# Performance work log

Hardware: AMD Instinct MI355X
Metric: run time of the kernel (lower is better)

The kernel has to match this reference:

```python
import jax, jax.numpy as jnp
import numpy as np

B, T, C = 8, 2048, 1024
H, S = 16, 64  # heads, head size (R=K=V=S)
HEAD_SIZE_DIVISOR = 8.0
EPS = 1e-5


def setup_inputs() -> dict:
    key = jax.random.key(0)
    ks = jax.random.split(key, 16)
    n = lambda k, shape, s=1.0: jax.random.normal(k, shape, dtype=jnp.float32) * s
    u = lambda k, shape: jax.random.uniform(k, shape, dtype=jnp.float32)
    w_scale = 0.02
    return {
        "xq": n(ks[0], (B, T, C)),
        "xk": n(ks[1], (B, T, C)),
        "xv": n(ks[2], (B, T, C)),
        "time_mix_k": u(ks[3], (1, 1, C)),
        "time_mix_v": u(ks[4], (1, 1, C)),
        "time_mix_r": u(ks[5], (1, 1, C)),
        "time_mix_g": u(ks[6], (1, 1, C)),
        "time_decay": n(ks[7], (H, S)),          # decay speed logits
        "time_faaaa": u(ks[8], (H, S)) * 0.5,     # per-channel bonus
        "Wr": n(ks[9], (C, C), w_scale),
        "Wk": n(ks[10], (C, C), w_scale),
        "Wv": n(ks[11], (C, C), w_scale),
        "Wg": n(ks[12], (C, C), w_scale),
        "Wo": n(ks[13], (C, C), w_scale),
        "ln_w": jnp.ones((C,), jnp.float32),
        "ln_b": jnp.zeros((C,), jnp.float32),
    }


def reference(xq, xk, xv, time_mix_k, time_mix_v, time_mix_r, time_mix_g,
              time_decay, time_faaaa, Wr, Wk, Wv, Wg, Wo, ln_w, ln_b):
    # Note: the torch forward ignores its xk/xv args and rebuilds them from xq.
    x = xq
    Bx, Tx, Cx = x.shape
    # time_shift: shift sequence right by 1, zero-pad first position
    xs = jnp.concatenate([jnp.zeros_like(x[:, :1]), x[:, :-1]], axis=1)
    mix = lambda m: x * m + xs * (1.0 - m)
    # projections (torch Linear: y = x @ W.T), split into heads
    r = (mix(time_mix_r) @ Wr.T).reshape(Bx, Tx, H, S)
    k = (mix(time_mix_k) @ Wk.T).reshape(Bx, Tx, H, S)
    v = (mix(time_mix_v) @ Wv.T).reshape(Bx, Tx, H, S)
    g = jax.nn.silu(mix(time_mix_g) @ Wg.T)  # (B, T, H*S)

    w = jnp.exp(-jnp.exp(time_decay))[None, :, :, None]  # (1,H,K,1) per-k-channel decay in (0,1)
    u = time_faaaa[None, :, :, None]                      # (1,H,K,1) bonus for current token

    def step(s, rkv):
        rt, kt, vt = rkv  # each (B, H, S)
        at = jnp.einsum('bhk,bhv->bhkv', kt, vt)          # outer product
        out = jnp.einsum('bhk,bhkv->bhv', rt, u * at + s)
        return at + w * s, out

    rkv = (jnp.swapaxes(r, 0, 1).swapaxes(1, 2).transpose(0, 1, 2, 3),) if False else None
    r_t = r.transpose(1, 0, 2, 3)  # (T, B, H, S)
    k_t = k.transpose(1, 0, 2, 3)
    v_t = v.transpose(1, 0, 2, 3)
    s0 = jnp.zeros((Bx, H, S, S), dtype=x.dtype)
    _, out = jax.lax.scan(step, s0, (r_t, k_t, v_t))  # out: (T, B, H, S)
    out = out.transpose(1, 0, 2, 3)  # (B, T, H, S)

    # GroupNorm with num_groups=H over channels H*S, applied to out/8
    y = out / HEAD_SIZE_DIVISOR
    mu = y.mean(axis=-1, keepdims=True)
    var = y.var(axis=-1, keepdims=True)
    y = (y - mu) / jnp.sqrt(var + EPS)
    y = y.reshape(Bx, Tx, H * S) * ln_w + ln_b

    return (y * g) @ Wo.T
```

## Files before the change

### kernel.cpp

```cpp
#include <hip/hip_runtime.h>
#include <stdint.h>

using bf16x8 = __attribute__((ext_vector_type(8))) __bf16;
using f32x4  = __attribute__((ext_vector_type(4))) float;

__device__ __forceinline__ unsigned short f2bf(float f) {
  unsigned u = __float_as_uint(f);
  u = u + 0x7FFFu + ((u >> 16) & 1u);
  return (unsigned short)(u >> 16);
}
__device__ __forceinline__ float bf2f(unsigned short h) {
  return __uint_as_float(((unsigned)h) << 16);
}
__device__ __forceinline__ void gload16(const void* g, void* l) {
  __builtin_amdgcn_global_load_lds((const __attribute__((address_space(1))) void*)g,
                                   (__attribute__((address_space(3))) void*)l, 16, 0, 0);
}

__global__ __launch_bounds__(256) void castw5_kernel(
    const float* __restrict__ w0, const float* __restrict__ w1,
    const float* __restrict__ w2, const float* __restrict__ w3,
    const float* __restrict__ w4, unsigned short* __restrict__ o) {
  const float* wsrc[5] = {w0, w1, w2, w3, w4};
  const float* w = wsrc[blockIdx.y];
  int i4 = blockIdx.x * 256 + threadIdx.x;
  float4 f = *(const float4*)(w + (size_t)i4 * 4);
  ushort4 u;
  u.x = f2bf(f.x); u.y = f2bf(f.y); u.z = f2bf(f.z); u.w = f2bf(f.w);
  *(ushort4*)(o + (size_t)blockIdx.y * 1048576 + (size_t)i4 * 4) = u;
}

__global__ __launch_bounds__(256) void mix1_kernel(const float* __restrict__ x,
                                                   const float* __restrict__ m,
                                                   unsigned short* __restrict__ amix) {
  int idx = blockIdx.x * 256 + threadIdx.x;
  int row = idx >> 8;
  int c0  = (idx & 255) << 2;
  size_t xoff = (size_t)row * 1024 + c0;
  float4 xv = *(const float4*)(x + xoff);
  float4 xs = make_float4(0.f, 0.f, 0.f, 0.f);
  if ((row & 2047) != 0) xs = *(const float4*)(x + xoff - 1024);
  float4 mm = *(const float4*)(m + c0);
  ushort4 u;
  u.x = f2bf(xv.x * mm.x + xs.x * (1.f - mm.x));
  u.y = f2bf(xv.y * mm.y + xs.y * (1.f - mm.y));
  u.z = f2bf(xv.z * mm.z + xs.z * (1.f - mm.z));
  u.w = f2bf(xv.w * mm.w + xs.w * (1.f - mm.w));
  *(ushort4*)(amix + xoff) = u;
}

__global__ __launch_bounds__(256) void gemm_kernel(
    const unsigned short* __restrict__ A,
    const unsigned short* __restrict__ W,
    unsigned short* __restrict__ Cbf,
    float* __restrict__ Cf,
    int do_silu, int f32out) {
  const int brow = blockIdx.y * 128;
  const int bcol = blockIdx.x * 128;
  const int t = threadIdx.x;
  const int lane = t & 63, wv = t >> 6;
  const int wr = wv >> 1, wc = wv & 1;
  const int lm = lane & 15, lk = lane >> 4;

  __shared__ __align__(16) unsigned short Al[128 * 32];
  __shared__ __align__(16) unsigned short Bl[128 * 32];

  f32x4 acc[4][4];
  const f32x4 z4 = {0.f, 0.f, 0.f, 0.f};
  #pragma unroll
  for (int mi = 0; mi < 4; ++mi)
    #pragma unroll
    for (int ni = 0; ni < 4; ++ni) acc[mi][ni] = z4;

  for (int kt = 0; kt < 32; ++kt) {
    __syncthreads();
    #pragma unroll
    for (int is = 0; is < 2; ++is) {
      int chunk = is * 256 + t;
      int r  = chunk >> 2;
      int c8 = (chunk & 3) << 3;
      int lb = (is * 256 + wv * 64) * 8;
      gload16(A + (size_t)(brow + r) * 1024 + kt * 32 + c8, &Al[lb]);
      gload16(W + (size_t)(bcol + r) * 1024 + kt * 32 + c8, &Bl[lb]);
    }
    __syncthreads();
    bf16x8 af[4], bfv[4];
    #pragma unroll
    for (int mi = 0; mi < 4; ++mi)
      af[mi] = *(const bf16x8*)&Al[(wr * 64 + mi * 16 + lm) * 32 + lk * 8];
    #pragma unroll
    for (int ni = 0; ni < 4; ++ni)
      bfv[ni] = *(const bf16x8*)&Bl[(wc * 64 + ni * 16 + lm) * 32 + lk * 8];
    #pragma unroll
    for (int mi = 0; mi < 4; ++mi)
      #pragma unroll
      for (int ni = 0; ni < 4; ++ni)
        acc[mi][ni] = __builtin_amdgcn_mfma_f32_16x16x32_bf16(af[mi], bfv[ni], acc[mi][ni], 0, 0, 0);
  }

  const int r0 = brow + wr * 64;
  const int c0 = bcol + wc * 64;
  #pragma unroll
  for (int mi = 0; mi < 4; ++mi) {
    #pragma unroll
    for (int ni = 0; ni < 4; ++ni) {
      #pragma unroll
      for (int rg = 0; rg < 4; ++rg) {
        int row = r0 + mi * 16 + lk * 4 + rg;
        int col = c0 + ni * 16 + lm;
        float v = acc[mi][ni][rg];
        if (f32out) {
          Cf[(size_t)row * 1024 + col] = v;
        } else {
          if (do_silu) v = v / (1.f + expf(-v));
          Cbf[(size_t)row * 1024 + col] = f2bf(v);
        }
      }
    }
  }
}

__global__ __launch_bounds__(256) void scan_pass1(
    const unsigned short* __restrict__ kg,
    const unsigned short* __restrict__ vg,
    const float* __restrict__ td,
    float* __restrict__ states) {
  const int c = blockIdx.x, h = blockIdx.y, b = blockIdx.z;
  const int t = threadIdx.x, lane = t & 63, wv = t >> 6;
  __shared__ __align__(16) unsigned short kwT[64 * 128];
  __shared__ __align__(16) unsigned short vT[64 * 128];

  const int a  = t & 7;
  const int d0 = a * 8;
  const int sb = t >> 3;
  float eta[8];
  #pragma unroll
  for (int j = 0; j < 8; ++j) eta[j] = expf(td[h * 64 + d0 + j]);
  const int t0 = c * 128;
  #pragma unroll
  for (int i = 0; i < 4; ++i) {
    int s = sb + 32 * i;
    size_t goff = ((size_t)(b * 2048 + t0 + s) * 16 + h) * 64 + d0;
    uint4 ku = *(const uint4*)(kg + goff);
    uint4 vu = *(const uint4*)(vg + goff);
    unsigned short kv[8] = {(unsigned short)(ku.x & 0xffff), (unsigned short)(ku.x >> 16),
                            (unsigned short)(ku.y & 0xffff), (unsigned short)(ku.y >> 16),
                            (unsigned short)(ku.z & 0xffff), (unsigned short)(ku.z >> 16),
                            (unsigned short)(ku.w & 0xffff), (unsigned short)(ku.w >> 16)};
    unsigned short vv[8] = {(unsigned short)(vu.x & 0xffff), (unsigned short)(vu.x >> 16),
                            (unsigned short)(vu.y & 0xffff), (unsigned short)(vu.y >> 16),
                            (unsigned short)(vu.z & 0xffff), (unsigned short)(vu.z >> 16),
                            (unsigned short)(vu.w & 0xffff), (unsigned short)(vu.w >> 16)};
    float p = -(float)(127 - s);
    int ss = s ^ (a << 3);
    #pragma unroll
    for (int j = 0; j < 8; ++j) {
      float wpow = expf(p * eta[j]);
      kwT[(d0 + j) * 128 + ss] = f2bf(bf2f(kv[j]) * wpow);
      vT [(d0 + j) * 128 + ss] = vv[j];
    }
  }
  __syncthreads();

  const int lm = lane & 15, lk = lane >> 4;
  const int aR = (wv * 2 + (lm >> 3)) & 7;
  f32x4 acc[4];
  const f32x4 z4 = {0.f, 0.f, 0.f, 0.f};
  #pragma unroll
  for (int ni = 0; ni < 4; ++ni) acc[ni] = z4;
  #pragma unroll
  for (int ks = 0; ks < 4; ++ks) {
    bf16x8 af = *(const bf16x8*)&kwT[(wv * 16 + lm) * 128 + (((ks * 4 + lk) ^ aR) << 3)];
    #pragma unroll
    for (int ni = 0; ni < 4; ++ni) {
      int aV = (ni * 2 + (lm >> 3)) & 7;
      bf16x8 bv = *(const bf16x8*)&vT[(ni * 16 + lm) * 128 + (((ks * 4 + lk) ^ aV) << 3)];
      acc[ni] = __builtin_amdgcn_mfma_f32_16x16x32_bf16(af, bv, acc[ni], 0, 0, 0);
    }
  }
  size_t base = (((size_t)(b * 16 + h) * 16 + c) * 64) * 64;
  #pragma unroll
  for (int ni = 0; ni < 4; ++ni)
    #pragma unroll
    for (int rg = 0; rg < 4; ++rg) {
      int row = wv * 16 + lk * 4 + rg;
      int col = ni * 16 + lm;
      states[base + (size_t)row * 64 + col] = acc[ni][rg];
    }
}

__global__ __launch_bounds__(256) void scan_pass2(const float* __restrict__ td,
                                                  float* __restrict__ states) {
  const int bh = blockIdx.x;
  const int h = bh & 15;
  const int t = threadIdx.x;
  float run[16], wl[16];
  #pragma unroll
  for (int i = 0; i < 16; ++i) {
    int kk = (t + i * 256) >> 6;
    wl[i] = expf(-128.f * expf(td[h * 64 + kk]));
    run[i] = 0.f;
  }
  size_t base0 = (size_t)bh * 16 * 4096;
  for (int c = 0; c < 16; ++c) {
    size_t base = base0 + (size_t)c * 4096;
    #pragma unroll
    for (int i = 0; i < 16; ++i) {
      float tmp = states[base + t + i * 256];
      states[base + t + i * 256] = run[i];
      run[i] = fmaf(wl[i], run[i], tmp);
    }
  }
}

__global__ __launch_bounds__(256) void scan_pass3(
    const unsigned short* __restrict__ rg,
    const unsigned short* __restrict__ kg,
    const unsigned short* __restrict__ vg,
    const float* __restrict__ td,
    const float* __restrict__ fa,
    const float* __restrict__ states,
    const float* __restrict__ lnw,
    const float* __restrict__ lnb,
    unsigned short* gbuf ) {
  const int c = blockIdx.x, h = blockIdx.y, b = blockIdx.z;
  const int t = threadIdx.x, lane = t & 63, wv = t >> 6;
  const int kq = lane & 3;
  const int jj = wv * 16 + (lane >> 2);
  float w_i[16], u_i[16], s_i[16];
  size_t sbase = (((size_t)(b * 16 + h) * 16 + c) * 64) * 64;
  #pragma unroll
  for (int i = 0; i < 16; ++i) {
    int kk = kq * 16 + i;
    w_i[i] = expf(-expf(td[h * 64 + kk]));
    u_i[i] = fa[h * 64 + kk];
    s_i[i] = states[sbase + (size_t)kk * 64 + jj];
  }
  __shared__ __align__(16) float rb[16][64];
  __shared__ __align__(16) float kb[16][64];
  __shared__ __align__(16) float vb[16][64];
  __shared__ __align__(16) float ob[16][64];
  const int t0 = c * 128;
  for (int q0 = 0; q0 < 128; q0 += 16) {
    __syncthreads();
    for (int ch = t; ch < 384; ch += 256) {
      int a = ch >> 7, rem = ch & 127;
      int q = rem >> 3, c8 = (rem & 7) << 3;
      const unsigned short* src = (a == 0) ? rg : ((a == 1) ? kg : vg);
      uint4 u = *(const uint4*)(src + ((size_t)(b * 2048 + t0 + q0 + q) * 16 + h) * 64 + c8);
      float* dst = (a == 0) ? &rb[q][c8] : ((a == 1) ? &kb[q][c8] : &vb[q][c8]);
      dst[0] = bf2f(u.x & 0xffff); dst[1] = bf2f(u.x >> 16);
      dst[2] = bf2f(u.y & 0xffff); dst[3] = bf2f(u.y >> 16);
      dst[4] = bf2f(u.z & 0xffff); dst[5] = bf2f(u.z >> 16);
      dst[6] = bf2f(u.w & 0xffff); dst[7] = bf2f(u.w >> 16);
    }
    __syncthreads();
    #pragma unroll
    for (int q = 0; q < 16; ++q) {
      float vj = vb[q][jj];
      const float4* rp = (const float4*)&rb[q][kq * 16];
      const float4* kp = (const float4*)&kb[q][kq * 16];
      float acc = 0.f;
      #pragma unroll
      for (int a4 = 0; a4 < 4; ++a4) {
        float4 r4 = rp[a4], k4 = kp[a4];
        { float kv = k4.x * vj; acc = fmaf(r4.x, fmaf(u_i[a4*4+0], kv, s_i[a4*4+0]), acc); s_i[a4*4+0] = fmaf(w_i[a4*4+0], s_i[a4*4+0], kv); }
        { float kv = k4.y * vj; acc = fmaf(r4.y, fmaf(u_i[a4*4+1], kv, s_i[a4*4+1]), acc); s_i[a4*4+1] = fmaf(w_i[a4*4+1], s_i[a4*4+1], kv); }
        { float kv = k4.z * vj; acc = fmaf(r4.z, fmaf(u_i[a4*4+2], kv, s_i[a4*4+2]), acc); s_i[a4*4+2] = fmaf(w_i[a4*4+2], s_i[a4*4+2], kv); }
        { float kv = k4.w * vj; acc = fmaf(r4.w, fmaf(u_i[a4*4+3], kv, s_i[a4*4+3]), acc); s_i[a4*4+3] = fmaf(w_i[a4*4+3], s_i[a4*4+3], kv); }
      }
      acc += __shfl_xor(acc, 1);
      acc += __shfl_xor(acc, 2);
      if (kq == 0) ob[q][jj] = acc;
    }
    __syncthreads();
    {
      int r  = wv * 4 + (lane >> 4);
      int c4 = (lane & 15) * 4;
      float4 y4 = *(const float4*)&ob[r][c4];
      y4.x *= 0.125f; y4.y *= 0.125f; y4.z *= 0.125f; y4.w *= 0.125f;
      float s1 = y4.x + y4.y + y4.z + y4.w;
      float s2 = y4.x * y4.x + y4.y * y4.y + y4.z * y4.z + y4.w * y4.w;
      #pragma unroll
      for (int d = 1; d < 16; d <<= 1) {
        s1 += __shfl_xor(s1, d);
        s2 += __shfl_xor(s2, d);
      }
      float mean = s1 * 0.015625f;
      float var  = s2 * 0.015625f - mean * mean;
      float rstd = rsqrtf(var + 1e-5f);
      float4 lw = *(const float4*)(lnw + h * 64 + c4);
      float4 lb = *(const float4*)(lnb + h * 64 + c4);
      size_t go = ((size_t)(b * 2048 + t0 + q0 + r) * 16 + h) * 64 + c4;
      uint2 gu = *(const uint2*)(gbuf + go);
      float g0 = bf2f(gu.x & 0xffff), g1 = bf2f(gu.x >> 16);
      float g2 = bf2f(gu.y & 0xffff), g3 = bf2f(gu.y >> 16);
      ushort4 o;
      o.x = f2bf(((y4.x - mean) * rstd * lw.x + lb.x) * g0);
      o.y = f2bf(((y4.y - mean) * rstd * lw.y + lb.y) * g1);
      o.z = f2bf(((y4.z - mean) * rstd * lw.z + lb.z) * g2);
      o.w = f2bf(((y4.w - mean) * rstd * lw.w + lb.w) * g3);
      *(ushort4*)(gbuf + go) = o;
    }
  }
}

extern "C" void kernel_launch(void* const* d_in, const int* in_sizes, int n_in,
                              void* d_out, int out_size, void* d_ws, size_t ws_size,
                              hipStream_t stream) {
  const float* xq  = (const float*)d_in[0];
  const float* tmk = (const float*)d_in[3];
  const float* tmv = (const float*)d_in[4];
  const float* tmr = (const float*)d_in[5];
  const float* tmg = (const float*)d_in[6];
  const float* td  = (const float*)d_in[7];
  const float* fa  = (const float*)d_in[8];
  const float* lnw = (const float*)d_in[14];
  const float* lnb = (const float*)d_in[15];

  char* ws = (char*)d_ws;
  unsigned short* WBF  = (unsigned short*)(ws);
  char*           SCR  = ws + 10485760ull;
  unsigned short* RKVG = (unsigned short*)(ws + 44040192ull);
  unsigned short* AMIX = (unsigned short*)SCR;
  float*          ST   = (float*)SCR;

  castw5_kernel<<<dim3(1024, 5), 256, 0, stream>>>(
      (const float*)d_in[9], (const float*)d_in[10], (const float*)d_in[11],
      (const float*)d_in[12], (const float*)d_in[13], WBF);

  const float* mixes[4] = {tmr, tmk, tmv, tmg};
  for (int z = 0; z < 4; ++z) {
    mix1_kernel<<<16384, 256, 0, stream>>>(xq, mixes[z], AMIX);
    gemm_kernel<<<dim3(8, 128), 256, 0, stream>>>(AMIX, WBF + (size_t)z * 1048576,
                                                  RKVG + (size_t)z * 16777216, (float*)nullptr,
                                                  (z == 3) ? 1 : 0, 0);
  }

  scan_pass1<<<dim3(16, 16, 8), 256, 0, stream>>>(RKVG + 16777216ull, RKVG + 33554432ull, td, ST);
  scan_pass2<<<128, 256, 0, stream>>>(td, ST);
  scan_pass3<<<dim3(16, 16, 8), 256, 0, stream>>>(RKVG, RKVG + 16777216ull, RKVG + 33554432ull,
                                                  td, fa, ST, lnw, lnb, RKVG + 50331648ull);

  gemm_kernel<<<dim3(8, 128), 256, 0, stream>>>(RKVG + 50331648ull, WBF + 4194304ull,
                                                (unsigned short*)nullptr, (float*)d_out, 0, 1);
}
```

Baseline: 748.1 us.

## Replace GEMM with 256x256-tile double-buffered 8-wave pipelined kernel

Replaces the 128x128, single-buffered GEMM with a 256x256 tile, 512-thread kernel. It uses K-steps of 64, double-buffered LDS with global_load_lds prefetch interleaved across four phases, s_setprio around MFMA bursts, and a block-index swizzle for L2 locality. The goal is to hide global-load latency behind MFMA work and raise arithmetic intensity for all five projection GEMMs. In exchange it uses 128 KB of LDS per block, more accumulator registers, and fine-grained vmcnt/barrier synchronisation that must be exactly right. The grid shrinks to 256 blocks, which may underfill the CUs.

After: 746.7 us. Within noise of the previous version (-0.2%).

```diff
diff --git a/kernel.cpp b/kernel.cpp
--- a/kernel.cpp
+++ b/kernel.cpp
@@ -49,59 +49,100 @@
   *(ushort4*)(amix + xoff) = u;
 }
 
-__global__ __launch_bounds__(256) void gemm_kernel(
+__global__ __launch_bounds__(512, 2) void gemm8p_kernel(
     const unsigned short* __restrict__ A,
     const unsigned short* __restrict__ W,
     unsigned short* __restrict__ Cbf,
     float* __restrict__ Cf,
     int do_silu, int f32out) {
-  const int brow = blockIdx.y * 128;
-  const int bcol = blockIdx.x * 128;
+  int orig = blockIdx.y * 4 + blockIdx.x;
+  int wg   = (orig & 7) * 32 + (orig >> 3);
+  const int bx = wg & 3, by = wg >> 2;
   const int t = threadIdx.x;
-  const int lane = t & 63, wv = t >> 6;
-  const int wr = wv >> 1, wc = wv & 1;
+  const int lane = t & 63, wid = t >> 6;
+  const int wr = wid >> 2, wc = wid & 3;
   const int lm = lane & 15, lk = lane >> 4;
 
-  __shared__ __align__(16) unsigned short Al[128 * 32];
-  __shared__ __align__(16) unsigned short Bl[128 * 32];
-
-  f32x4 acc[4][4];
+  __shared__ __align__(16) unsigned short Abuf[2][16384];
+  __shared__ __align__(16) unsigned short Bbuf[2][16384];
+
+  const unsigned short* gA = A + ((size_t)by * 256 + (t >> 3)) * 1024 + (t & 7) * 8;
+  const unsigned short* gB = W + ((size_t)bx * 256 + (t >> 3)) * 1024 + (t & 7) * 8;
+  unsigned short* dA = &Abuf[0][0] + t * 8;
+  unsigned short* dB = &Bbuf[0][0] + t * 8;
+
+#define STA(buf, kt, r) gload16(gA + (size_t)(r) * 65536 + (kt) * 64, dA + (buf) * 16384 + (r) * 4096)
+#define STB(buf, kt, r) gload16(gB + (size_t)(r) * 65536 + (kt) * 64, dB + (buf) * 16384 + (r) * 4096)
+
+  f32x4 acc[8][4];
   const f32x4 z4 = {0.f, 0.f, 0.f, 0.f};
   #pragma unroll
-  for (int mi = 0; mi < 4; ++mi)
+  for (int mi = 0; mi < 8; ++mi)
     #pragma unroll
     for (int ni = 0; ni < 4; ++ni) acc[mi][ni] = z4;
 
-  for (int kt = 0; kt < 32; ++kt) {
-    __syncthreads();
-    #pragma unroll
-    for (int is = 0; is < 2; ++is) {
-      int chunk = is * 256 + t;
-      int r  = chunk >> 2;
-      int c8 = (chunk & 3) << 3;
-      int lb = (is * 256 + wv * 64) * 8;
-      gload16(A + (size_t)(brow + r) * 1024 + kt * 32 + c8, &Al[lb]);
-      gload16(W + (size_t)(bcol + r) * 1024 + kt * 32 + c8, &Bl[lb]);
-    }
-    __syncthreads();
-    bf16x8 af[4], bfv[4];
-    #pragma unroll
-    for (int mi = 0; mi < 4; ++mi)
-      af[mi] = *(const bf16x8*)&Al[(wr * 64 + mi * 16 + lm) * 32 + lk * 8];
-    #pragma unroll
-    for (int ni = 0; ni < 4; ++ni)
-      bfv[ni] = *(const bf16x8*)&Bl[(wc * 64 + ni * 16 + lm) * 32 + lk * 8];
-    #pragma unroll
-    for (int mi = 0; mi < 4; ++mi)
-      #pragma unroll
-      for (int ni = 0; ni < 4; ++ni)
-        acc[mi][ni] = __builtin_amdgcn_mfma_f32_16x16x32_bf16(af[mi], bfv[ni], acc[mi][ni], 0, 0, 0);
-  }
-
-  const int r0 = brow + wr * 64;
-  const int c0 = bcol + wc * 64;
-  #pragma unroll
-  for (int mi = 0; mi < 4; ++mi) {
+  STB(0, 0, 0); STB(0, 0, 2); STB(0, 0, 1); STB(0, 0, 3);
+  STA(0, 0, 0); STA(0, 0, 2); STA(0, 0, 1); STA(0, 0, 3);
+  asm volatile("s_waitcnt vmcnt(2)" ::: "memory");
+  __builtin_amdgcn_s_barrier();
+
+  const int aoff = (wr * 128 + lm) * 64 + lk * 8;
+  const int boff = (wc * 64 + lm) * 64 + lk * 8;
+
+  for (int tt = 0; tt < 16; ++tt) {
+    const int b = tt & 1;
+    const unsigned short* Ab = &Abuf[b][0];
+    const unsigned short* Bb = &Bbuf[b][0];
+    bf16x8 bfr[4][2];
+    #pragma unroll
+    for (int p = 0; p < 4; ++p) {
+      if (tt < 15) {
+        const int b2 = b ^ 1, k1 = tt + 1;
+        if (p == 0)      { STB(b2, k1, 0); STB(b2, k1, 2); }
+        else if (p == 1) { STB(b2, k1, 1); STB(b2, k1, 3); }
+        else if (p == 2) { STA(b2, k1, 0); STA(b2, k1, 2); }
+        else             { STA(b2, k1, 1); STA(b2, k1, 3); }
+      }
+      if (p == 0) {
+        #pragma unroll
+        for (int ni = 0; ni < 4; ++ni)
+          #pragma unroll
+          for (int ks = 0; ks < 2; ++ks)
+            bfr[ni][ks] = *(const bf16x8*)&Bb[boff + ni * 1024 + ks * 32];
+      }
+      bf16x8 af[2][2];
+      #pragma unroll
+      for (int j = 0; j < 2; ++j)
+        #pragma unroll
+        for (int ks = 0; ks < 2; ++ks)
+          af[j][ks] = *(const bf16x8*)&Ab[aoff + (2 * p + j) * 1024 + ks * 32];
+      __builtin_amdgcn_s_barrier();
+      __builtin_amdgcn_s_setprio(1);
+      #pragma unroll
+      for (int j = 0; j < 2; ++j)
+        #pragma unroll
+        for (int ni = 0; ni < 4; ++ni)
+          #pragma unroll
+          for (int ks = 0; ks < 2; ++ks)
+            acc[2 * p + j][ni] = __builtin_amdgcn_mfma_f32_16x16x32_bf16(
+                af[j][ks], bfr[ni][ks], acc[2 * p + j][ni], 0, 0, 0);
+      __builtin_amdgcn_s_setprio(0);
+      if (p == 1) {
+        if (tt == 15) asm volatile("s_waitcnt vmcnt(0)" ::: "memory");
+        else          asm volatile("s_waitcnt vmcnt(4)" ::: "memory");
+      } else if (p == 3) {
+        asm volatile("s_waitcnt vmcnt(2)" ::: "memory");
+      }
+      __builtin_amdgcn_s_barrier();
+    }
+  }
+#undef STA
+#undef STB
+
+  const int r0 = by * 256 + wr * 128;
+  const int c0 = bx * 256 + wc * 64;
+  #pragma unroll
+  for (int mi = 0; mi < 8; ++mi) {
     #pragma unroll
     for (int ni = 0; ni < 4; ++ni) {
       #pragma unroll
@@ -332,9 +373,9 @@
   const float* mixes[4] = {tmr, tmk, tmv, tmg};
   for (int z = 0; z < 4; ++z) {
     mix1_kernel<<<16384, 256, 0, stream>>>(xq, mixes[z], AMIX);
-    gemm_kernel<<<dim3(8, 128), 256, 0, stream>>>(AMIX, WBF + (size_t)z * 1048576,
-                                                  RKVG + (size_t)z * 16777216, (float*)nullptr,
-                                                  (z == 3) ? 1 : 0, 0);
+    gemm8p_kernel<<<dim3(4, 64), 512, 0, stream>>>(AMIX, WBF + (size_t)z * 1048576,
+                                                   RKVG + (size_t)z * 16777216, (float*)nullptr,
+                                                   (z == 3) ? 1 : 0, 0);
   }
 
   scan_pass1<<<dim3(16, 16, 8), 256, 0, stream>>>(RKVG + 16777216ull, RKVG + 33554432ull, td, ST);
@@ -342,6 +383,6 @@
   scan_pass3<<<dim3(16, 16, 8), 256, 0, stream>>>(RKVG, RKVG + 16777216ull, RKVG + 33554432ull,
                                                   td, fa, ST, lnw, lnb, RKVG + 50331648ull);
 
-  gemm_kernel<<<dim3(8, 128), 256, 0, stream>>>(RKVG + 50331648ull, WBF + 4194304ull,
-                                                (unsigned short*)nullptr, (float*)d_out, 0, 1);
-}
+  gemm8p_kernel<<<dim3(4, 64), 512, 0, stream>>>(RKVG + 50331648ull, WBF + 4194304ull,
+                                                 (unsigned short*)nullptr, (float*)d_out, 0, 1);
+}
```
